# Performance work log

Hardware: AMD Instinct MI355X
Metric: run time of the kernel (lower is better)

The kernel has to match this reference:

```python
import math
import jax, jax.numpy as jnp
import numpy as np

N = 65536   # total nodes across episodes
H = 512     # hidden size
B = 4096    # number of episodes / decoding items
M = 32      # max neighbors (padded ragged valid_actions)


def setup_inputs() -> dict:
    key = jax.random.key(0)
    ks = jax.random.split(key, 9)
    s = 1.0 / math.sqrt(H)
    return {
        "h_static": jax.random.normal(ks[0], (N, H), jnp.float32),
        "h_dynamic": jax.random.normal(ks[1], (N, H), jnp.float32),
        "Ws_kvl": jax.random.normal(ks[2], (H, 3 * H), jnp.float32) * s,
        "Wd_kvl": jax.random.normal(ks[3], (H, 3 * H), jnp.float32) * s,
        "Wq": jax.random.normal(ks[4], (H, H), jnp.float32) * s,
        "batch": jax.random.randint(ks[5], (N,), 0, B, jnp.int32),
        "current_nodes": jax.random.randint(ks[6], (B,), 0, N),
        "neigh_idx": jax.random.randint(ks[7], (B, M), 0, N),
        "lengths": jax.random.randint(ks[8], (B,), 0, M + 1),
    }


def reference(h_static, h_dynamic, Ws_kvl, Wd_kvl, Wq, batch, current_nodes, neigh_idx, lengths):
    # precompute(): static KVL projection (full 3H GEMM then chunk, as in torch)
    kvl_s = h_static @ Ws_kvl            # [N, 3H]
    K_s = kvl_s[:, :H]
    # forward_batch(): dynamic projection
    kvl_d = h_dynamic @ Wd_kvl           # [N, 3H]
    K_d = kvl_d[:, :H]
    K = K_s + K_d                        # [N, H]  (V is computed but unused for outputs)
    q = (h_static[current_nodes] + h_dynamic[current_nodes]) @ Wq  # [B, H]

    # padded ragged neighbor attention (replaces the Python loop over B)
    Kn = K[neigh_idx]                                        # [B, M, H]
    compat = jnp.einsum('bmh,bh->bm', Kn, q) / math.sqrt(H)  # [B, M]
    mask = jnp.arange(M)[None, :] < lengths[:, None]         # [B, M]
    NEG = jnp.float32(-1e9)
    logits = jnp.where(mask, compat, NEG)

    # categorical sampling via Gumbel-max (Categorical(logits).sample())
    u = jax.random.uniform(jax.random.key(1), (B, M), jnp.float32, 1e-8, 1.0)
    g = -jnp.log(-jnp.log(u))
    idx = jnp.argmax(logits + g, axis=-1)                    # [B]

    logp = jax.nn.log_softmax(logits, axis=-1)               # [B, M]
    lp = jnp.take_along_axis(logp, idx[:, None], axis=1)[:, 0]
    actions = jnp.take_along_axis(neigh_idx, idx[:, None], axis=1)[:, 0]

    # empty neighbor list -> stay at current node, log_prob 0 (matches torch branch)
    nonempty = lengths > 0
    actions = jnp.where(nonempty, actions, current_nodes)
    lp = jnp.where(nonempty, lp, jnp.float32(0.0))
    return actions, lp
```

## Files before the change

### kernel.cpp

```cpp
#include <hip/hip_runtime.h>
#include <cstdint>
#include <cstddef>

#define HDIM 512
#define NM 32
#define NBATCH 4096
#define NNODE 65536
#define CAP 16

__device__ __forceinline__ unsigned rotl32(unsigned x, unsigned d) {
  return (x << d) | (x >> (32u - d));
}

__device__ __forceinline__ void threefry2x32(unsigned& x0, unsigned& x1) {
  const unsigned ks0 = 0u, ks1 = 1u, ks2 = 0x1BD11BDBu;
  x0 += ks0; x1 += ks1;
#define TF_RND(r) { x0 += x1; x1 = rotl32(x1, (r)); x1 ^= x0; }
  TF_RND(13) TF_RND(15) TF_RND(26) TF_RND(6)
  x0 += ks1; x1 += ks2 + 1u;
  TF_RND(17) TF_RND(29) TF_RND(16) TF_RND(24)
  x0 += ks2; x1 += ks0 + 2u;
  TF_RND(13) TF_RND(15) TF_RND(26) TF_RND(6)
  x0 += ks0; x1 += ks1 + 3u;
  TF_RND(17) TF_RND(29) TF_RND(16) TF_RND(24)
  x0 += ks1; x1 += ks2 + 4u;
  TF_RND(13) TF_RND(15) TF_RND(26) TF_RND(6)
  x0 += ks2; x1 += ks0 + 5u;
#undef TF_RND
}

__global__ __launch_bounds__(256) void zero_cnt(int* __restrict__ cnt,
                                                int* __restrict__ ovf_cnt) {
  const int t = blockIdx.x * 256 + threadIdx.x;
  ((int4*)cnt)[t] = make_int4(0, 0, 0, 0);
  if (t == 0) *ovf_cnt = 0;
}

__global__ void gather_hc(const float* __restrict__ hs,
                          const float* __restrict__ hd,
                          const int* __restrict__ cur,
                          float* __restrict__ Hc) {
  const int b = blockIdx.x;
  const int t = threadIdx.x;
  const int n = cur[b];
  const float4 a = ((const float4*)(hs + (size_t)n * HDIM))[t];
  const float4 c = ((const float4*)(hd + (size_t)n * HDIM))[t];
  float4 r;
  r.x = a.x + c.x; r.y = a.y + c.y; r.z = a.z + c.z; r.w = a.w + c.w;
  ((float4*)(Hc + (size_t)b * HDIM))[t] = r;
}

__global__ __launch_bounds__(256) void gemm_b1(const float* __restrict__ Ws,
                                               const float* __restrict__ Wd,
                                               const float* __restrict__ Wq,
                                               float* __restrict__ M2T) {
  constexpr int BK = 16, LDT = 68;
  __shared__ float Ast[BK][LDT];
  __shared__ float Bst[BK][LDT];
  const int tid = threadIdx.x;
  const int row0 = blockIdx.y * 64;
  const int col0 = blockIdx.x * 64;
  const float* Abase = (row0 < 512) ? Ws : Wd;
  const int arow0 = (row0 < 512) ? row0 : row0 - 512;
  const int tx = tid & 15, ty = tid >> 4;
  const int lr = tid >> 2, lc = (tid & 3) * 4;
  float acc[4][4] = {};
  for (int k0 = 0; k0 < 512; k0 += BK) {
    float4 va = *(const float4*)(Abase + (size_t)(arow0 + lr) * 1536 + k0 + lc);
    float4 vb = *(const float4*)(Wq + (size_t)(col0 + lr) * 512 + k0 + lc);
    Ast[lc + 0][lr] = va.x; Ast[lc + 1][lr] = va.y;
    Ast[lc + 2][lr] = va.z; Ast[lc + 3][lr] = va.w;
    Bst[lc + 0][lr] = vb.x; Bst[lc + 1][lr] = vb.y;
    Bst[lc + 2][lr] = vb.z; Bst[lc + 3][lr] = vb.w;
    __syncthreads();
#pragma unroll
    for (int k = 0; k < BK; ++k) {
      float4 a4 = *(const float4*)&Ast[k][ty * 4];
      float4 b4 = *(const float4*)&Bst[k][tx * 4];
      float a[4] = {a4.x, a4.y, a4.z, a4.w};
      float bb[4] = {b4.x, b4.y, b4.z, b4.w};
#pragma unroll
      for (int i = 0; i < 4; ++i)
#pragma unroll
        for (int j = 0; j < 4; ++j) acc[i][j] += a[i] * bb[j];
    }
    __syncthreads();
  }
#pragma unroll
  for (int i = 0; i < 4; ++i) {
    float4 o;
    o.x = acc[i][0]; o.y = acc[i][1]; o.z = acc[i][2]; o.w = acc[i][3];
    *(float4*)(M2T + (size_t)(row0 + ty * 4 + i) * 512 + col0 + tx * 4) = o;
  }
}

__global__ __launch_bounds__(256) void gemm_v(const float* __restrict__ A,
                                              const float* __restrict__ Bm,
                                              float* __restrict__ C) {
  constexpr int BK = 32, LDT = 68;
  __shared__ float Ast[BK][LDT];
  __shared__ float Bst[BK][LDT];
  const int tid = threadIdx.x;
  const int row0 = blockIdx.y * 64;
  const int col0 = blockIdx.x * 64;
  const int tx = tid & 15, ty = tid >> 4;
  const int lr = tid >> 3;
  const int lc = (tid & 7) * 4;
  float acc[4][4] = {};
  for (int k0 = 0; k0 < 512; k0 += BK) {
    const float4 va0 = *(const float4*)(A + (size_t)(row0 + lr) * 512 + k0 + lc);
    const float4 va1 = *(const float4*)(A + (size_t)(row0 + lr + 32) * 512 + k0 + lc);
    const float4 vb0 = *(const float4*)(Bm + (size_t)(col0 + lr) * 512 + k0 + lc);
    const float4 vb1 = *(const float4*)(Bm + (size_t)(col0 + lr + 32) * 512 + k0 + lc);
    Ast[lc + 0][lr] = va0.x; Ast[lc + 1][lr] = va0.y;
    Ast[lc + 2][lr] = va0.z; Ast[lc + 3][lr] = va0.w;
    Ast[lc + 0][lr + 32] = va1.x; Ast[lc + 1][lr + 32] = va1.y;
    Ast[lc + 2][lr + 32] = va1.z; Ast[lc + 3][lr + 32] = va1.w;
    Bst[lc + 0][lr] = vb0.x; Bst[lc + 1][lr] = vb0.y;
    Bst[lc + 2][lr] = vb0.z; Bst[lc + 3][lr] = vb0.w;
    Bst[lc + 0][lr + 32] = vb1.x; Bst[lc + 1][lr + 32] = vb1.y;
    Bst[lc + 2][lr + 32] = vb1.z; Bst[lc + 3][lr + 32] = vb1.w;
    __syncthreads();
#pragma unroll
    for (int k = 0; k < BK; ++k) {
      const float4 a4 = *(const float4*)&Ast[k][ty * 4];
      const float4 b4 = *(const float4*)&Bst[k][tx * 4];
      const float a[4] = {a4.x, a4.y, a4.z, a4.w};
      const float bb[4] = {b4.x, b4.y, b4.z, b4.w};
#pragma unroll
      for (int i = 0; i < 4; ++i)
#pragma unroll
        for (int j = 0; j < 4; ++j) acc[i][j] += a[i] * bb[j];
    }
    __syncthreads();
  }
#pragma unroll
  for (int i = 0; i < 4; ++i) {
    float4 o;
    o.x = acc[i][0]; o.y = acc[i][1]; o.z = acc[i][2]; o.w = acc[i][3];
    *(float4*)(C + (size_t)(row0 + ty * 4 + i) * 1024 + col0 + tx * 4) = o;
  }
}

__global__ __launch_bounds__(256) void build_index(
    const int* __restrict__ neigh, const int* __restrict__ lens,
    int* __restrict__ cnt, int* __restrict__ bucket,
    int* __restrict__ ovf_cnt, int* __restrict__ ovf_list) {
  const int t = blockIdx.x * 256 + threadIdx.x;
  const int b = t >> 5, m = t & 31;
  if (m < lens[b]) {
    const int n = neigh[t];
    const int slot = atomicAdd(&cnt[n], 1);
    if (slot < CAP) bucket[n * CAP + slot] = t;
    else { const int o = atomicAdd(ovf_cnt, 1); ovf_list[o] = t; }
  }
}

__global__ __launch_bounds__(256) void stream_compat(
    const float* __restrict__ hs, const float* __restrict__ hd,
    const float* __restrict__ V, const int* __restrict__ cnt,
    const int* __restrict__ bucket, float* __restrict__ compat) {
  const int n = blockIdx.x * 4 + (threadIdx.x >> 6);
  const int lane = threadIdx.x & 63;
  const int c = cnt[n];
  if (c == 0) return;
  const float4* a4 = (const float4*)(hs + (size_t)n * HDIM);
  const float4* c4 = (const float4*)(hd + (size_t)n * HDIM);
  const float4 a0 = a4[lane * 2], a1 = a4[lane * 2 + 1];
  const float4 b0 = c4[lane * 2], b1 = c4[lane * 2 + 1];
  const int cc = (c < CAP) ? c : CAP;
  for (int e = 0; e < cc; ++e) {
    const int t = bucket[n * CAP + e];
    const int b = t >> 5;
    const float4* vrow = (const float4*)(V + (size_t)b * (2 * HDIM));
    const float4 w0 = vrow[lane * 2], w1 = vrow[lane * 2 + 1];
    const float4 u0 = vrow[128 + lane * 2], u1 = vrow[128 + lane * 2 + 1];
    float acc = a0.x * w0.x + a0.y * w0.y + a0.z * w0.z + a0.w * w0.w
              + a1.x * w1.x + a1.y * w1.y + a1.z * w1.z + a1.w * w1.w
              + b0.x * u0.x + b0.y * u0.y + b0.z * u0.z + b0.w * u0.w
              + b1.x * u1.x + b1.y * u1.y + b1.z * u1.z + b1.w * u1.w;
#pragma unroll
    for (int off = 32; off >= 1; off >>= 1) acc += __shfl_xor(acc, off);
    if (lane == 0) compat[t] = acc;
  }
}

__global__ __launch_bounds__(256) void ovf_compat(
    const float* __restrict__ hs, const float* __restrict__ hd,
    const float* __restrict__ V, const int* __restrict__ ovf_cnt,
    const int* __restrict__ ovf_list, const int* __restrict__ neigh,
    float* __restrict__ compat) {
  const int nw = *ovf_cnt;
  const int lane = threadIdx.x & 63;
  for (int e = blockIdx.x * 4 + (threadIdx.x >> 6); e < nw; e += gridDim.x * 4) {
    const int t = ovf_list[e];
    const int b = t >> 5;
    const int n = neigh[t];
    const float4* a4 = (const float4*)(hs + (size_t)n * HDIM);
    const float4* c4 = (const float4*)(hd + (size_t)n * HDIM);
    const float4 a0 = a4[lane * 2], a1 = a4[lane * 2 + 1];
    const float4 b0 = c4[lane * 2], b1 = c4[lane * 2 + 1];
    const float4* vrow = (const float4*)(V + (size_t)b * (2 * HDIM));
    const float4 w0 = vrow[lane * 2], w1 = vrow[lane * 2 + 1];
    const float4 u0 = vrow[128 + lane * 2], u1 = vrow[128 + lane * 2 + 1];
    float acc = a0.x * w0.x + a0.y * w0.y + a0.z * w0.z + a0.w * w0.w
              + a1.x * w1.x + a1.y * w1.y + a1.z * w1.z + a1.w * w1.w
              + b0.x * u0.x + b0.y * u0.y + b0.z * u0.z + b0.w * u0.w
              + b1.x * u1.x + b1.y * u1.y + b1.z * u1.z + b1.w * u1.w;
#pragma unroll
    for (int off = 32; off >= 1; off >>= 1) acc += __shfl_xor(acc, off);
    if (lane == 0) compat[t] = acc;
  }
}

__global__ __launch_bounds__(256) void finalize_kernel(
    const float* __restrict__ compat, const int* __restrict__ neigh,
    const int* __restrict__ lengths, const int* __restrict__ cur,
    float* __restrict__ out) {
  const int b = blockIdx.x * 4 + (threadIdx.x >> 6);
  const int tid = threadIdx.x & 63;
  const int len = lengths[b];
  const bool valid = tid < NM;
  const float NEGMAX = -3.402823466e38f;
  float logit = NEGMAX;
  if (valid) {
    const float cm = compat[b * NM + tid] / 22.62741699796952f;
    logit = (tid < len) ? cm : -1e9f;
  }
  float z = NEGMAX;
  int zi = 1 << 20;
  if (valid) {
    const unsigned i_lo = (unsigned)b * 32u + (unsigned)tid;
    unsigned x0 = 0u;
    unsigned x1 = i_lo;
    threefry2x32(x0, x1);
    const unsigned bits = x0 ^ x1;
    const float fu = __uint_as_float((bits >> 9) | 0x3f800000u) - 1.0f;
    const float uu = fmaxf(1e-8f, fu + 1e-8f);
    const float g = -logf(-logf(uu));
    z = logit + g;
    zi = tid;
  }
#pragma unroll
  for (int off = 32; off >= 1; off >>= 1) {
    const float oz = __shfl_xor(z, off);
    const int oi = __shfl_xor(zi, off);
    if (oz > z || (oz == z && oi < zi)) { z = oz; zi = oi; }
  }
  float ml = logit;
#pragma unroll
  for (int off = 32; off >= 1; off >>= 1) ml = fmaxf(ml, __shfl_xor(ml, off));
  float ex = valid ? expf(logit - ml) : 0.f;
#pragma unroll
  for (int off = 32; off >= 1; off >>= 1) ex += __shfl_xor(ex, off);
  const float lsel = __shfl(logit, zi);
  if (tid == 0) {
    float lp = lsel - ml - logf(ex);
    int act = neigh[b * NM + zi];
    if (len <= 0) { act = cur[b]; lp = 0.f; }
    out[b] = (float)act;
    out[NBATCH + b] = lp;
  }
}

extern "C" void kernel_launch(void* const* d_in, const int* in_sizes, int n_in,
                              void* d_out, int out_size, void* d_ws, size_t ws_size,
                              hipStream_t stream) {
  const float* hs = (const float*)d_in[0];
  const float* hd = (const float*)d_in[1];
  const float* Ws = (const float*)d_in[2];
  const float* Wd = (const float*)d_in[3];
  const float* Wq = (const float*)d_in[4];
  const int* cur = (const int*)d_in[6];
  const int* neigh = (const int*)d_in[7];
  const int* lens = (const int*)d_in[8];
  float* out = (float*)d_out;

  char* ws = (char*)d_ws;
  size_t off = 0;
  int* cnt = (int*)(ws + off);        off += (size_t)NNODE * 4;
  int* ovf_cnt = (int*)(ws + off);    off += 256;
  int* bucket = (int*)(ws + off);     off += (size_t)NNODE * CAP * 4;
  int* ovf_list = (int*)(ws + off);   off += (size_t)NBATCH * NM * 4;
  float* compat = (float*)(ws + off); off += (size_t)NBATCH * NM * 4;
  float* Hc = (float*)(ws + off);     off += (size_t)NBATCH * HDIM * 4;
  float* M2T = (float*)(ws + off);    off += (size_t)1024 * 512 * 4;
  float* V = (float*)(ws + off);      off += (size_t)NBATCH * 2 * HDIM * 4;

  hipLaunchKernelGGL(zero_cnt, dim3(64), dim3(256), 0, stream, cnt, ovf_cnt);
  hipLaunchKernelGGL(build_index, dim3(NBATCH * NM / 256), dim3(256), 0, stream,
                     neigh, lens, cnt, bucket, ovf_cnt, ovf_list);
  hipLaunchKernelGGL(gemm_b1, dim3(8, 16), dim3(256), 0, stream, Ws, Wd, Wq, M2T);
  hipLaunchKernelGGL(gather_hc, dim3(NBATCH), dim3(128), 0, stream, hs, hd, cur, Hc);
  hipLaunchKernelGGL(gemm_v, dim3(16, 64), dim3(256), 0, stream, Hc, M2T, V);
  hipLaunchKernelGGL(stream_compat, dim3(NNODE / 4), dim3(256), 0, stream,
                     hs, hd, V, cnt, bucket, compat);
  hipLaunchKernelGGL(ovf_compat, dim3(32), dim3(256), 0, stream,
                     hs, hd, V, ovf_cnt, ovf_list, neigh, compat);
  hipLaunchKernelGGL(finalize_kernel, dim3(NBATCH / 4), dim3(256), 0, stream,
                     compat, neigh, lens, cur, out);
}
```

Before: 174.5 us.

## Fuse node gather into GEMM and overflow pass into streaming compat kernel

The gather of h_static+h_dynamic at current nodes now happens inside the V GEMM's A-tile load, removing the Hc buffer and its kernel. The overflow compat kernel is merged into stream_compat, with its first 32 blocks handling overflow entries. Streamed node rows use nontemporal loads to avoid polluting cache. This removes two launches and one intermediate round trip, at the cost of redundant gathered A loads across column blocks.

Result: faster. 168.1 us (-3.7%).

```diff
diff --git a/kernel.cpp b/kernel.cpp
--- a/kernel.cpp
+++ b/kernel.cpp
@@ -7,6 +7,8 @@
 #define NBATCH 4096
 #define NNODE 65536
 #define CAP 16
+
+typedef float v4f __attribute__((ext_vector_type(4)));
 
 __device__ __forceinline__ unsigned rotl32(unsigned x, unsigned d) {
   return (x << d) | (x >> (32u - d));
@@ -34,20 +36,6 @@
   const int t = blockIdx.x * 256 + threadIdx.x;
   ((int4*)cnt)[t] = make_int4(0, 0, 0, 0);
   if (t == 0) *ovf_cnt = 0;
-}
-
-__global__ void gather_hc(const float* __restrict__ hs,
-                          const float* __restrict__ hd,
-                          const int* __restrict__ cur,
-                          float* __restrict__ Hc) {
-  const int b = blockIdx.x;
-  const int t = threadIdx.x;
-  const int n = cur[b];
-  const float4 a = ((const float4*)(hs + (size_t)n * HDIM))[t];
-  const float4 c = ((const float4*)(hd + (size_t)n * HDIM))[t];
-  float4 r;
-  r.x = a.x + c.x; r.y = a.y + c.y; r.z = a.z + c.z; r.w = a.w + c.w;
-  ((float4*)(Hc + (size_t)b * HDIM))[t] = r;
 }
 
 __global__ __launch_bounds__(256) void gemm_b1(const float* __restrict__ Ws,
@@ -94,7 +82,9 @@
   }
 }
 
-__global__ __launch_bounds__(256) void gemm_v(const float* __restrict__ A,
+__global__ __launch_bounds__(256) void gemm_v(const float* __restrict__ hs,
+                                              const float* __restrict__ hd,
+                                              const int* __restrict__ cur,
                                               const float* __restrict__ Bm,
                                               float* __restrict__ C) {
   constexpr int BK = 32, LDT = 68;
@@ -106,16 +96,20 @@
   const int tx = tid & 15, ty = tid >> 4;
   const int lr = tid >> 3;
   const int lc = (tid & 7) * 4;
+  const size_t n0 = (size_t)cur[row0 + lr] * HDIM;
+  const size_t n1 = (size_t)cur[row0 + lr + 32] * HDIM;
   float acc[4][4] = {};
   for (int k0 = 0; k0 < 512; k0 += BK) {
-    const float4 va0 = *(const float4*)(A + (size_t)(row0 + lr) * 512 + k0 + lc);
-    const float4 va1 = *(const float4*)(A + (size_t)(row0 + lr + 32) * 512 + k0 + lc);
+    const float4 s0 = *(const float4*)(hs + n0 + k0 + lc);
+    const float4 d0 = *(const float4*)(hd + n0 + k0 + lc);
+    const float4 s1 = *(const float4*)(hs + n1 + k0 + lc);
+    const float4 d1 = *(const float4*)(hd + n1 + k0 + lc);
     const float4 vb0 = *(const float4*)(Bm + (size_t)(col0 + lr) * 512 + k0 + lc);
     const float4 vb1 = *(const float4*)(Bm + (size_t)(col0 + lr + 32) * 512 + k0 + lc);
-    Ast[lc + 0][lr] = va0.x; Ast[lc + 1][lr] = va0.y;
-    Ast[lc + 2][lr] = va0.z; Ast[lc + 3][lr] = va0.w;
-    Ast[lc + 0][lr + 32] = va1.x; Ast[lc + 1][lr + 32] = va1.y;
-    Ast[lc + 2][lr + 32] = va1.z; Ast[lc + 3][lr + 32] = va1.w;
+    Ast[lc + 0][lr] = s0.x + d0.x; Ast[lc + 1][lr] = s0.y + d0.y;
+    Ast[lc + 2][lr] = s0.z + d0.z; Ast[lc + 3][lr] = s0.w + d0.w;
+    Ast[lc + 0][lr + 32] = s1.x + d1.x; Ast[lc + 1][lr + 32] = s1.y + d1.y;
+    Ast[lc + 2][lr + 32] = s1.z + d1.z; Ast[lc + 3][lr + 32] = s1.w + d1.w;
     Bst[lc + 0][lr] = vb0.x; Bst[lc + 1][lr] = vb0.y;
     Bst[lc + 2][lr] = vb0.z; Bst[lc + 3][lr] = vb0.w;
     Bst[lc + 0][lr + 32] = vb1.x; Bst[lc + 1][lr + 32] = vb1.y;
@@ -159,57 +153,56 @@
 __global__ __launch_bounds__(256) void stream_compat(
     const float* __restrict__ hs, const float* __restrict__ hd,
     const float* __restrict__ V, const int* __restrict__ cnt,
-    const int* __restrict__ bucket, float* __restrict__ compat) {
+    const int* __restrict__ bucket, const int* __restrict__ ovf_cnt,
+    const int* __restrict__ ovf_list, const int* __restrict__ neigh,
+    float* __restrict__ compat) {
   const int n = blockIdx.x * 4 + (threadIdx.x >> 6);
   const int lane = threadIdx.x & 63;
   const int c = cnt[n];
-  if (c == 0) return;
-  const float4* a4 = (const float4*)(hs + (size_t)n * HDIM);
-  const float4* c4 = (const float4*)(hd + (size_t)n * HDIM);
-  const float4 a0 = a4[lane * 2], a1 = a4[lane * 2 + 1];
-  const float4 b0 = c4[lane * 2], b1 = c4[lane * 2 + 1];
-  const int cc = (c < CAP) ? c : CAP;
-  for (int e = 0; e < cc; ++e) {
-    const int t = bucket[n * CAP + e];
-    const int b = t >> 5;
-    const float4* vrow = (const float4*)(V + (size_t)b * (2 * HDIM));
-    const float4 w0 = vrow[lane * 2], w1 = vrow[lane * 2 + 1];
-    const float4 u0 = vrow[128 + lane * 2], u1 = vrow[128 + lane * 2 + 1];
-    float acc = a0.x * w0.x + a0.y * w0.y + a0.z * w0.z + a0.w * w0.w
-              + a1.x * w1.x + a1.y * w1.y + a1.z * w1.z + a1.w * w1.w
-              + b0.x * u0.x + b0.y * u0.y + b0.z * u0.z + b0.w * u0.w
-              + b1.x * u1.x + b1.y * u1.y + b1.z * u1.z + b1.w * u1.w;
-#pragma unroll
-    for (int off = 32; off >= 1; off >>= 1) acc += __shfl_xor(acc, off);
-    if (lane == 0) compat[t] = acc;
-  }
-}
-
-__global__ __launch_bounds__(256) void ovf_compat(
-    const float* __restrict__ hs, const float* __restrict__ hd,
-    const float* __restrict__ V, const int* __restrict__ ovf_cnt,
-    const int* __restrict__ ovf_list, const int* __restrict__ neigh,
-    float* __restrict__ compat) {
-  const int nw = *ovf_cnt;
-  const int lane = threadIdx.x & 63;
-  for (int e = blockIdx.x * 4 + (threadIdx.x >> 6); e < nw; e += gridDim.x * 4) {
-    const int t = ovf_list[e];
-    const int b = t >> 5;
-    const int n = neigh[t];
-    const float4* a4 = (const float4*)(hs + (size_t)n * HDIM);
-    const float4* c4 = (const float4*)(hd + (size_t)n * HDIM);
-    const float4 a0 = a4[lane * 2], a1 = a4[lane * 2 + 1];
-    const float4 b0 = c4[lane * 2], b1 = c4[lane * 2 + 1];
-    const float4* vrow = (const float4*)(V + (size_t)b * (2 * HDIM));
-    const float4 w0 = vrow[lane * 2], w1 = vrow[lane * 2 + 1];
-    const float4 u0 = vrow[128 + lane * 2], u1 = vrow[128 + lane * 2 + 1];
-    float acc = a0.x * w0.x + a0.y * w0.y + a0.z * w0.z + a0.w * w0.w
-              + a1.x * w1.x + a1.y * w1.y + a1.z * w1.z + a1.w * w1.w
-              + b0.x * u0.x + b0.y * u0.y + b0.z * u0.z + b0.w * u0.w
-              + b1.x * u1.x + b1.y * u1.y + b1.z * u1.z + b1.w * u1.w;
-#pragma unroll
-    for (int off = 32; off >= 1; off >>= 1) acc += __shfl_xor(acc, off);
-    if (lane == 0) compat[t] = acc;
+  if (c != 0) {
+    const v4f* a4 = (const v4f*)(hs + (size_t)n * HDIM);
+    const v4f* c4 = (const v4f*)(hd + (size_t)n * HDIM);
+    const v4f a0 = __builtin_nontemporal_load(a4 + lane * 2);
+    const v4f a1 = __builtin_nontemporal_load(a4 + lane * 2 + 1);
+    const v4f b0 = __builtin_nontemporal_load(c4 + lane * 2);
+    const v4f b1 = __builtin_nontemporal_load(c4 + lane * 2 + 1);
+    const int cc = (c < CAP) ? c : CAP;
+    for (int e = 0; e < cc; ++e) {
+      const int t = bucket[n * CAP + e];
+      const int b = t >> 5;
+      const float4* vrow = (const float4*)(V + (size_t)b * (2 * HDIM));
+      const float4 w0 = vrow[lane * 2], w1 = vrow[lane * 2 + 1];
+      const float4 u0 = vrow[128 + lane * 2], u1 = vrow[128 + lane * 2 + 1];
+      float acc = a0.x * w0.x + a0.y * w0.y + a0.z * w0.z + a0.w * w0.w
+                + a1.x * w1.x + a1.y * w1.y + a1.z * w1.z + a1.w * w1.w
+                + b0.x * u0.x + b0.y * u0.y + b0.z * u0.z + b0.w * u0.w
+                + b1.x * u1.x + b1.y * u1.y + b1.z * u1.z + b1.w * u1.w;
+#pragma unroll
+      for (int off = 32; off >= 1; off >>= 1) acc += __shfl_xor(acc, off);
+      if (lane == 0) compat[t] = acc;
+    }
+  }
+  if (blockIdx.x < 32) {
+    const int nw = *ovf_cnt;
+    for (int e = blockIdx.x * 4 + (threadIdx.x >> 6); e < nw; e += 128) {
+      const int t = ovf_list[e];
+      const int b = t >> 5;
+      const int nn = neigh[t];
+      const float4* a4 = (const float4*)(hs + (size_t)nn * HDIM);
+      const float4* c4 = (const float4*)(hd + (size_t)nn * HDIM);
+      const float4 a0 = a4[lane * 2], a1 = a4[lane * 2 + 1];
+      const float4 b0 = c4[lane * 2], b1 = c4[lane * 2 + 1];
+      const float4* vrow = (const float4*)(V + (size_t)b * (2 * HDIM));
+      const float4 w0 = vrow[lane * 2], w1 = vrow[lane * 2 + 1];
+      const float4 u0 = vrow[128 + lane * 2], u1 = vrow[128 + lane * 2 + 1];
+      float acc = a0.x * w0.x + a0.y * w0.y + a0.z * w0.z + a0.w * w0.w
+                + a1.x * w1.x + a1.y * w1.y + a1.z * w1.z + a1.w * w1.w
+                + b0.x * u0.x + b0.y * u0.y + b0.z * u0.z + b0.w * u0.w
+                + b1.x * u1.x + b1.y * u1.y + b1.z * u1.z + b1.w * u1.w;
+#pragma unroll
+      for (int off = 32; off >= 1; off >>= 1) acc += __shfl_xor(acc, off);
+      if (lane == 0) compat[t] = acc;
+    }
   }
 }
 
@@ -283,7 +276,6 @@
   int* bucket = (int*)(ws + off);     off += (size_t)NNODE * CAP * 4;
   int* ovf_list = (int*)(ws + off);   off += (size_t)NBATCH * NM * 4;
   float* compat = (float*)(ws + off); off += (size_t)NBATCH * NM * 4;
-  float* Hc = (float*)(ws + off);     off += (size_t)NBATCH * HDIM * 4;
   float* M2T = (float*)(ws + off);    off += (size_t)1024 * 512 * 4;
   float* V = (float*)(ws + off);      off += (size_t)NBATCH * 2 * HDIM * 4;
 
@@ -291,12 +283,9 @@
   hipLaunchKernelGGL(build_index, dim3(NBATCH * NM / 256), dim3(256), 0, stream,
                      neigh, lens, cnt, bucket, ovf_cnt, ovf_list);
   hipLaunchKernelGGL(gemm_b1, dim3(8, 16), dim3(256), 0, stream, Ws, Wd, Wq, M2T);
-  hipLaunchKernelGGL(gather_hc, dim3(NBATCH), dim3(128), 0, stream, hs, hd, cur, Hc);
-  hipLaunchKernelGGL(gemm_v, dim3(16, 64), dim3(256), 0, stream, Hc, M2T, V);
+  hipLaunchKernelGGL(gemm_v, dim3(16, 64), dim3(256), 0, stream, hs, hd, cur, M2T, V);
   hipLaunchKernelGGL(stream_compat, dim3(NNODE / 4), dim3(256), 0, stream,
-                     hs, hd, V, cnt, bucket, compat);
-  hipLaunchKernelGGL(ovf_compat, dim3(32), dim3(256), 0, stream,
-                     hs, hd, V, ovf_cnt, ovf_list, neigh, compat);
+                     hs, hd, V, cnt, bucket, ovf_cnt, ovf_list, neigh, compat);
   hipLaunchKernelGGL(finalize_kernel, dim3(NBATCH / 4), dim3(256), 0, stream,
                      compat, neigh, lens, cur, out);
 }
```
